# Kernel tuning notes

Measured on AMD Instinct MI355X. Metric: run time of the kernel, lower is better.

The kernel has to match this reference:

```python
import jax, jax.numpy as jnp
import numpy as np

B, T, DIM, NH = 2, 2048, 1024, 16
HD = DIM // NH  # 64


def setup_inputs() -> dict:
    key = jax.random.key(0)
    ks = jax.random.split(key, 5)
    x = jax.random.normal(ks[0], (B, T, DIM), dtype=jnp.float32)
    # realistic RoPE tables (any float tables work; use true rotary angles)
    inv_freq = 1.0 / (10000.0 ** (jnp.arange(0, HD, 2, dtype=jnp.float32) / HD))  # [HD/2]
    ang = jnp.arange(T, dtype=jnp.float32)[:, None] * inv_freq[None, :]           # [T, HD/2]
    ang = jnp.repeat(ang, 2, axis=-1)                                             # [T, HD] interleaved pairs
    sin = jnp.sin(ang)[None, None]  # [1,1,T,HD]
    cos = jnp.cos(ang)[None, None]
    W_qkv = jax.random.normal(ks[1], (DIM, 3 * DIM), dtype=jnp.float32) * (DIM ** -0.5)
    W_proj = jax.random.normal(ks[2], (DIM, DIM), dtype=jnp.float32) * (DIM ** -0.5)
    return {"x": x, "sin": sin, "cos": cos, "W_qkv": W_qkv, "W_proj": W_proj}


def _rope(x, sin, cos):
    # x: [B,H,T,D]; sin/cos: [1,1,T,D]
    x1, x2 = x[..., ::2], x[..., 1::2]
    xr = jnp.stack((-x2, x1), axis=-1).reshape(x.shape)  # interleave (-x2, x1)
    return x * cos + xr * sin


def reference(x, sin, cos, W_qkv, W_proj):
    Bx, Tx, C = x.shape
    nh, hd = NH, C // NH
    qkv = x @ W_qkv                                   # [B,T,3C]
    q, k, v = jnp.split(qkv, 3, axis=-1)
    to_bhtd = lambda t: t.reshape(Bx, Tx, nh, hd).transpose(0, 2, 1, 3)
    q, k, v = to_bhtd(q), to_bhtd(k), to_bhtd(v)      # [B,H,T,D]
    q = _rope(q, sin[:, :, :Tx], cos[:, :, :Tx])
    k = _rope(k, sin[:, :, :Tx], cos[:, :, :Tx])
    scale = 1.0 / jnp.sqrt(jnp.asarray(hd, dtype=x.dtype))
    scores = jnp.einsum('bhqd,bhkd->bhqk', q, k) * scale
    causal = jnp.tril(jnp.ones((Tx, Tx), dtype=bool))
    scores = jnp.where(causal, scores, jnp.finfo(scores.dtype).min)
    attn = jax.nn.softmax(scores, axis=-1)
    y = jnp.einsum('bhqk,bhkd->bhqd', attn, v)        # [B,H,T,D]
    y = y.transpose(0, 2, 1, 3).reshape(Bx, Tx, C)
    return y @ W_proj
```

## Files before the change

kernel.cpp:

```cpp
#include <hip/hip_runtime.h>


typedef float  f32x4   __attribute__((ext_vector_type(4)));
typedef float  f32x16  __attribute__((ext_vector_type(16)));
typedef __bf16 bf16x8  __attribute__((ext_vector_type(8)));
typedef short  short8  __attribute__((ext_vector_type(8)));
typedef unsigned uint2v __attribute__((ext_vector_type(2)));
typedef unsigned uint4v __attribute__((ext_vector_type(4)));

#define Bb   2
#define Tt   2048
#define DIMc 1024
#define NHh  16
#define HDd  64

__device__ __forceinline__ short f2bf(float f) {
    unsigned u = __builtin_bit_cast(unsigned, f);
    u += 0x7fffu + ((u >> 16) & 1u);
    return (short)(u >> 16);
}

__device__ __forceinline__ f32x4 mfma16(short8 a, short8 b, f32x4 c) {
    return __builtin_amdgcn_mfma_f32_16x16x32_bf16(
        __builtin_bit_cast(bf16x8, a), __builtin_bit_cast(bf16x8, b), c, 0, 0, 0);
}

__device__ __forceinline__ f32x16 mfma32(short8 a, short8 b, f32x16 c) {
    return __builtin_amdgcn_mfma_f32_32x32x16_bf16(
        __builtin_bit_cast(bf16x8, a), __builtin_bit_cast(bf16x8, b), c, 0, 0, 0);
}

__device__ __forceinline__ unsigned cvtpk(float lo, float hi) {
    unsigned r;
    asm("v_cvt_pk_bf16_f32 %0, %1, %2" : "=v"(r) : "v"(lo), "v"(hi));
    return r;
}

__device__ __forceinline__ void gl_lds16(const void* g, void* l) {
    __builtin_amdgcn_global_load_lds(
        (const __attribute__((address_space(1))) unsigned int*)g,
        (__attribute__((address_space(3))) unsigned int*)l, 16, 0, 0);
}

__global__ __launch_bounds__(256) void convX(const float* __restrict__ X,
                                             short* __restrict__ Xb)
{
    size_t i = ((size_t)blockIdx.x * 256 + threadIdx.x) * 8;
    float4 a = *(const float4*)(X + i);
    float4 b = *(const float4*)(X + i + 4);
    short8 s;
    s[0] = f2bf(a.x); s[1] = f2bf(a.y); s[2] = f2bf(a.z); s[3] = f2bf(a.w);
    s[4] = f2bf(b.x); s[5] = f2bf(b.y); s[6] = f2bf(b.z); s[7] = f2bf(b.w);
    *(short8*)(Xb + i) = s;
}

__global__ __launch_bounds__(256) void convT(const float* __restrict__ W,
                                             short* __restrict__ Wt, int N)
{
    __shared__ float L[64][65];
    const int kb = blockIdx.x * 64, nb = blockIdx.y * 64;
    const int tid = threadIdx.x;
#pragma unroll
    for (int it = 0; it < 4; it++) {
        int kk = it * 16 + (tid >> 4), c = (tid & 15) * 4;
        float4 v = *(const float4*)(W + (size_t)(kb + kk) * N + nb + c);
        L[c + 0][kk] = v.x; L[c + 1][kk] = v.y;
        L[c + 2][kk] = v.z; L[c + 3][kk] = v.w;
    }
    __syncthreads();
#pragma unroll
    for (int it = 0; it < 2; it++) {
        int n = it * 32 + (tid >> 3), ks = (tid & 7) * 8;
        short8 s;
#pragma unroll
        for (int j = 0; j < 8; j++) s[j] = f2bf(L[n][ks + j]);
        *(short8*)(Wt + (size_t)(nb + n) * 1024 + kb + ks) = s;
    }
}

__global__ __launch_bounds__(256, 6) void qkv_rope(
    const short* __restrict__ A, const short* __restrict__ Bt,
    const float* __restrict__ Sn, const float* __restrict__ Cs,
    short* __restrict__ Qo, short* __restrict__ Ko, short* __restrict__ Vt)
{
    __shared__ __align__(16) short LP[64 * 64 + 128 * 64];
    short (*As)[64] = (short(*)[64])LP;
    short (*Bs)[64] = (short(*)[64])(LP + 64 * 64);

    const int bm = blockIdx.x, bn = blockIdx.y;
    const int tid = threadIdx.x;
    const int wv = tid >> 6, lane = tid & 63, g = lane >> 4, l16 = lane & 15;
    const int wr = wv >> 1, wc = wv & 1;
    const int sw = l16 & 7;

    f32x4 acc[2][4];
#pragma unroll
    for (int i = 0; i < 2; i++)
#pragma unroll
        for (int j = 0; j < 4; j++) acc[i][j] = (f32x4){0.f, 0.f, 0.f, 0.f};

    const int sr = tid >> 3, c8 = tid & 7;
    const int gc8 = (c8 ^ (sr & 7)) << 3;
    const short* pA = A  + (size_t)(bm * 64  + sr) * 1024 + gc8;
    const short* pB = Bt + (size_t)(bn * 128 + sr) * 1024 + gc8;

    for (int k0 = 0; k0 < 1024; k0 += 64) {
        gl_lds16(pA + k0,             &As[sr][c8 << 3]);
        gl_lds16(pA + k0 + 32 * 1024, &As[32 + sr][c8 << 3]);
        gl_lds16(pB + k0,             &Bs[sr][c8 << 3]);
        gl_lds16(pB + k0 + 32 * 1024, &Bs[32 + sr][c8 << 3]);
        gl_lds16(pB + k0 + 64 * 1024, &Bs[64 + sr][c8 << 3]);
        gl_lds16(pB + k0 + 96 * 1024, &Bs[96 + sr][c8 << 3]);
        __syncthreads();
#pragma unroll
        for (int ks = 0; ks < 2; ks++) {
            short8 af[2], bfr[4];
#pragma unroll
            for (int mt = 0; mt < 2; mt++)
                af[mt]  = *(const short8*)&As[wr * 32 + mt * 16 + l16][((ks * 4 + g) ^ sw) << 3];
#pragma unroll
            for (int nt = 0; nt < 4; nt++)
                bfr[nt] = *(const short8*)&Bs[wc * 64 + nt * 16 + l16][((ks * 4 + g) ^ sw) << 3];
#pragma unroll
            for (int mt = 0; mt < 2; mt++)
#pragma unroll
                for (int nt = 0; nt < 4; nt++) acc[mt][nt] = mfma16(af[mt], bfr[nt], acc[mt][nt]);
        }
        __syncthreads();
    }

    if (bn >= 16) {
        short (*T)[72] = (short(*)[72])LP;
        const int b  = bm >> 5;
        const int t0 = (bm * 64) & 2047;
        const int nbase = (bn - 16) * 128;
#pragma unroll
        for (int ch = 0; ch < 4; ++ch) {
            __syncthreads();
            if (wc == (ch >> 1)) {
#pragma unroll
                for (int ntl = 0; ntl < 2; ++ntl) {
                    int nt = (ch & 1) * 2 + ntl;
#pragma unroll
                    for (int mt = 0; mt < 2; ++mt)
#pragma unroll
                        for (int r = 0; r < 4; ++r)
                            T[ntl * 16 + l16][wr * 32 + mt * 16 + g * 4 + r] =
                                f2bf(acc[mt][nt][r]);
                }
            }
            __syncthreads();
            int row = tid >> 3, cc8 = (tid & 7) * 8;
            int nn = nbase + ch * 32 + row;
            int h = nn >> 6, d = nn & 63;
            short8 v0 = *(const short8*)&T[row][cc8];
            size_t base = (((size_t)(b * 16 + h) * 64 + d) << 11) + t0 + cc8;
            *(short8*)(Vt + base) = v0;
        }
    } else {
#pragma unroll
        for (int mt = 0; mt < 2; mt++)
#pragma unroll
            for (int nt = 0; nt < 4; nt++)
#pragma unroll
                for (int r = 0; r < 4; r++) {
                    int m = bm * 64 + wr * 32 + mt * 16 + g * 4 + r;
                    int n = bn * 128 + wc * 64 + nt * 16 + l16;
                    float val = acc[mt][nt][r];
                    float partner = __shfl_xor(val, 1, 64);
                    int b = m >> 11, t = m & 2047;
                    int sec = n >> 10, nn = n & 1023;
                    int h = nn >> 6, d = nn & 63;
                    float sv = Sn[t * 64 + d], cv = Cs[t * 64 + d];
                    float ro = (d & 1) ? fmaf(val, cv, partner * sv)
                                       : fmaf(val, cv, -partner * sv);
                    short* dst = (sec == 0) ? Qo : Ko;
                    dst[(((size_t)(b * 16 + h) << 11) + t) * 64 + d] = f2bf(ro);
                }
    }
}

__global__ __launch_bounds__(64, 4) void attn(
    const short* __restrict__ Q, const short* __restrict__ K,
    const short* __restrict__ V, short* __restrict__ Y)
{
    const int id = blockIdx.x;
    const int bh = id >> 6;
    const int qw = ((id & 63) + ((id >> 8) << 3)) & 63;
    const int lane = threadIdx.x;
    const int l5 = lane & 31, hi = lane >> 5;
    const int q0 = qw * 32;
    const int qabs = q0 + l5;

    const short* Qb = Q + (size_t)bh * Tt * 64;
    const short* Kb = K + (size_t)bh * Tt * 64;
    const short* Vb = V + (size_t)bh * 64 * Tt;

    short8 qf[4];
#pragma unroll
    for (int c = 0; c < 4; c++)
        qf[c] = *(const short8*)(Qb + (size_t)(q0 + l5) * 64 + c * 16 + hi * 8);

    f32x16 o0, o1;
    float lsum = 0.f;
#pragma unroll
    for (int r = 0; r < 16; r++) { o0[r] = 0.f; o1[r] = 0.f; }

    const int nsteps = qw + 1;
    for (int s = 0; s < nsteps; ++s) {
        const int k0 = s * 32;
        const short* kp = Kb + (size_t)(k0 + l5) * 64 + hi * 8;
        short8 kf0 = *(const short8*)(kp);
        short8 kf1 = *(const short8*)(kp + 16);
        short8 kf2 = *(const short8*)(kp + 32);
        short8 kf3 = *(const short8*)(kp + 48);
        const short* vp = Vb + (size_t)l5 * Tt + k0 + hi * 8;
        short8 vf00 = *(const short8*)(vp);
        short8 vf01 = *(const short8*)(vp + 16);
        short8 vf10 = *(const short8*)(vp + 32 * Tt);
        short8 vf11 = *(const short8*)(vp + 32 * Tt + 16);

        f32x16 st;
#pragma unroll
        for (int r = 0; r < 16; r++) st[r] = 0.f;
        st = mfma32(kf0, qf[0], st);
        st = mfma32(kf1, qf[1], st);
        st = mfma32(kf2, qf[2], st);
        st = mfma32(kf3, qf[3], st);

        float p[16];
        if (s < nsteps - 1) {
#pragma unroll
            for (int r = 0; r < 16; r++)
                p[r] = __expf(fmaf(st[r], 0.125f, -10.f));
        } else {
#pragma unroll
            for (int r = 0; r < 16; r++) {
                int key = k0 + (r & 3) + 8 * (r >> 2) + 4 * hi;
                p[r] = (key <= qabs) ? __expf(fmaf(st[r], 0.125f, -10.f)) : 0.f;
            }
        }
#pragma unroll
        for (int r = 0; r < 16; r += 4)
            lsum += (p[r] + p[r + 1]) + (p[r + 2] + p[r + 3]);

        unsigned w[8];
#pragma unroll
        for (int t = 0; t < 4; t++) {
            w[2 * t]     = cvtpk(p[4 * t],     p[4 * t + 1]);
            w[2 * t + 1] = cvtpk(p[4 * t + 2], p[4 * t + 3]);
        }
        uint2v s0 = __builtin_amdgcn_permlane32_swap(w[0], w[2], false, false);
        uint2v s1 = __builtin_amdgcn_permlane32_swap(w[1], w[3], false, false);
        uint2v s2 = __builtin_amdgcn_permlane32_swap(w[4], w[6], false, false);
        uint2v s3 = __builtin_amdgcn_permlane32_swap(w[5], w[7], false, false);
        uint4v u0 = {s0[0], s1[0], s0[1], s1[1]};
        uint4v u1 = {s2[0], s3[0], s2[1], s3[1]};
        short8 pa0 = __builtin_bit_cast(short8, u0);
        short8 pa1 = __builtin_bit_cast(short8, u1);

        o0 = mfma32(pa0, vf00, o0);
        o0 = mfma32(pa1, vf01, o0);
        o1 = mfma32(pa0, vf10, o1);
        o1 = mfma32(pa1, vf11, o1);
    }

    lsum += __shfl_xor(lsum, 32, 64);
    float inv = 1.0f / lsum;
    const int b = bh >> 4, h = bh & 15;
#pragma unroll
    for (int r = 0; r < 16; r++) {
        int ql = (r & 3) + 8 * (r >> 2) + 4 * hi;
        float iv = __shfl(inv, ql, 64);
        size_t row = ((size_t)(b * Tt + q0 + ql)) * DIMc + h * 64;
        Y[row + l5]      = f2bf(o0[r] * iv);
        Y[row + 32 + l5] = f2bf(o1[r] * iv);
    }
}

__global__ __launch_bounds__(256, 4) void proj(
    const short* __restrict__ A, const short* __restrict__ Bt, float* __restrict__ O)
{
    __shared__ __align__(16) short As[64][64];
    __shared__ __align__(16) short Bs[64][64];
    const int bm = blockIdx.x, bn = blockIdx.y;
    const int tid = threadIdx.x;
    const int wv = tid >> 6, lane = tid & 63, g = lane >> 4, l16 = lane & 15;
    const int wr = wv >> 1, wc = wv & 1;
    const int sw = l16 & 7;

    f32x4 acc[2][2];
#pragma unroll
    for (int i = 0; i < 2; i++)
#pragma unroll
        for (int j = 0; j < 2; j++) acc[i][j] = (f32x4){0.f, 0.f, 0.f, 0.f};

    const int sr = tid >> 3, c8 = tid & 7;
    const int gc8 = (c8 ^ (sr & 7)) << 3;
    const short* pA = A  + (size_t)(bm * 64 + sr) * 1024 + gc8;
    const short* pB = Bt + (size_t)(bn * 64 + sr) * 1024 + gc8;

    for (int k0 = 0; k0 < 1024; k0 += 64) {
        gl_lds16(pA + k0,             &As[sr][c8 << 3]);
        gl_lds16(pA + k0 + 32 * 1024, &As[32 + sr][c8 << 3]);
        gl_lds16(pB + k0,             &Bs[sr][c8 << 3]);
        gl_lds16(pB + k0 + 32 * 1024, &Bs[32 + sr][c8 << 3]);
        __syncthreads();
#pragma unroll
        for (int ks = 0; ks < 2; ks++) {
            short8 af[2], bfr[2];
#pragma unroll
            for (int mt = 0; mt < 2; mt++)
                af[mt]  = *(const short8*)&As[wr * 32 + mt * 16 + l16][((ks * 4 + g) ^ sw) << 3];
#pragma unroll
            for (int nt = 0; nt < 2; nt++)
                bfr[nt] = *(const short8*)&Bs[wc * 32 + nt * 16 + l16][((ks * 4 + g) ^ sw) << 3];
#pragma unroll
            for (int mt = 0; mt < 2; mt++)
#pragma unroll
                for (int nt = 0; nt < 2; nt++) acc[mt][nt] = mfma16(af[mt], bfr[nt], acc[mt][nt]);
        }
        __syncthreads();
    }

#pragma unroll
    for (int mt = 0; mt < 2; mt++)
#pragma unroll
        for (int nt = 0; nt < 2; nt++)
#pragma unroll
            for (int r = 0; r < 4; r++) {
                int m = bm * 64 + wr * 32 + mt * 16 + g * 4 + r;
                int n = bn * 64 + wc * 32 + nt * 16 + l16;
                O[(size_t)m * 1024 + n] = acc[mt][nt][r];
            }
}

extern "C" void kernel_launch(void* const* d_in, const int* in_sizes, int n_in,
                              void* d_out, int out_size, void* d_ws, size_t ws_size,
                              hipStream_t stream)
{
    const float* x     = (const float*)d_in[0];
    const float* sn    = (const float*)d_in[1];
    const float* cs    = (const float*)d_in[2];
    const float* wqkv  = (const float*)d_in[3];
    const float* wproj = (const float*)d_in[4];
    float* out = (float*)d_out;

    char* ws = (char*)d_ws;
    const size_t MB = 1024 * 1024;
    short* q   = (short*)(ws);
    short* k   = (short*)(ws + 8  * MB);
    short* vt  = (short*)(ws + 16 * MB);
    short* y   = (short*)(ws + 24 * MB);
    short* xb  = (short*)(ws + 32 * MB);
    short* wqt = (short*)(ws + 40 * MB);
    short* wpt = (short*)(ws + 46 * MB);

    convX<<<2048, 256, 0, stream>>>(x, xb);
    convT<<<dim3(16, 48), 256, 0, stream>>>(wqkv, wqt, 3072);
    convT<<<dim3(16, 16), 256, 0, stream>>>(wproj, wpt, 1024);
    qkv_rope<<<dim3(64, 24), 256, 0, stream>>>(xb, wqt, sn, cs, q, k, vt);
    attn<<<dim3(Tt / 32 * Bb * NHh), 64, 0, stream>>>(q, k, vt, y);
    proj<<<dim3(64, 16), 256, 0, stream>>>(y, wpt, out);
}
```

Before: 220.9 us.

## Share K/V tiles in LDS across four waves with balanced causal pairing

```diff
diff --git a/kernel.cpp b/kernel.cpp
--- a/kernel.cpp
+++ b/kernel.cpp
@@ -180,102 +180,142 @@
     }
 }
 
-__global__ __launch_bounds__(64, 4) void attn(
+__global__ __launch_bounds__(256, 2) void attn(
     const short* __restrict__ Q, const short* __restrict__ K,
     const short* __restrict__ V, short* __restrict__ Y)
 {
-    const int id = blockIdx.x;
-    const int bh = id >> 6;
-    const int qw = ((id & 63) + ((id >> 8) << 3)) & 63;
-    const int lane = threadIdx.x;
+    __shared__ __align__(16) short Ks[2][64][64];
+    __shared__ __align__(16) short Vs[2][64][64];
+
+    const int bid = blockIdx.x;
+    const int xcd = bid & 7, idx = bid >> 3;
+    const int bh = xcd * 4 + (idx >> 4);
+    const int qb = idx & 15;
+    const int tid = threadIdx.x;
+    const int wv = tid >> 6, lane = tid & 63;
     const int l5 = lane & 31, hi = lane >> 5;
-    const int q0 = qw * 32;
-    const int qabs = q0 + l5;
+    const int swl = l5 & 7;
 
     const short* Qb = Q + (size_t)bh * Tt * 64;
     const short* Kb = K + (size_t)bh * Tt * 64;
     const short* Vb = V + (size_t)bh * 64 * Tt;
-
-    short8 qf[4];
-#pragma unroll
-    for (int c = 0; c < 4; c++)
-        qf[c] = *(const short8*)(Qb + (size_t)(q0 + l5) * 64 + c * 16 + hi * 8);
-
-    f32x16 o0, o1;
-    float lsum = 0.f;
-#pragma unroll
-    for (int r = 0; r < 16; r++) { o0[r] = 0.f; o1[r] = 0.f; }
-
-    const int nsteps = qw + 1;
-    for (int s = 0; s < nsteps; ++s) {
-        const int k0 = s * 32;
-        const short* kp = Kb + (size_t)(k0 + l5) * 64 + hi * 8;
-        short8 kf0 = *(const short8*)(kp);
-        short8 kf1 = *(const short8*)(kp + 16);
-        short8 kf2 = *(const short8*)(kp + 32);
-        short8 kf3 = *(const short8*)(kp + 48);
-        const short* vp = Vb + (size_t)l5 * Tt + k0 + hi * 8;
-        short8 vf00 = *(const short8*)(vp);
-        short8 vf01 = *(const short8*)(vp + 16);
-        short8 vf10 = *(const short8*)(vp + 32 * Tt);
-        short8 vf11 = *(const short8*)(vp + 32 * Tt + 16);
-
-        f32x16 st;
-#pragma unroll
-        for (int r = 0; r < 16; r++) st[r] = 0.f;
-        st = mfma32(kf0, qf[0], st);
-        st = mfma32(kf1, qf[1], st);
-        st = mfma32(kf2, qf[2], st);
-        st = mfma32(kf3, qf[3], st);
-
-        float p[16];
-        if (s < nsteps - 1) {
-#pragma unroll
-            for (int r = 0; r < 16; r++)
-                p[r] = __expf(fmaf(st[r], 0.125f, -10.f));
-        } else {
-#pragma unroll
-            for (int r = 0; r < 16; r++) {
-                int key = k0 + (r & 3) + 8 * (r >> 2) + 4 * hi;
-                p[r] = (key <= qabs) ? __expf(fmaf(st[r], 0.125f, -10.f)) : 0.f;
+    const int b = bh >> 4, h = bh & 15;
+
+    const int srow0 = wv * 16 + (lane >> 3);
+    const int sgp   = lane & 7;
+
+    auto stage = [&](int s, int buf) {
+        const int k0 = s * 64;
+#pragma unroll
+        for (int j = 0; j < 2; j++) {
+            int row = srow0 + j * 8;
+            int gl = sgp ^ (row & 7);
+            gl_lds16(Kb + (size_t)(k0 + row) * 64 + gl * 8, &Ks[buf][row][sgp << 3]);
+            gl_lds16(Vb + (size_t)row * Tt + k0 + gl * 8,   &Vs[buf][row][sgp << 3]);
+        }
+    };
+
+    auto run_phase = [&](int qw, int smax_blk) {
+        const int q0 = qw * 32, qabs = q0 + l5;
+        const int smax_w = qw >> 1;
+
+        short8 qf[4];
+#pragma unroll
+        for (int c = 0; c < 4; c++)
+            qf[c] = *(const short8*)(Qb + (size_t)(q0 + l5) * 64 + c * 16 + hi * 8);
+
+        f32x16 o0, o1;
+        float lsum = 0.f;
+#pragma unroll
+        for (int r = 0; r < 16; r++) { o0[r] = 0.f; o1[r] = 0.f; }
+
+        stage(0, 0);
+        __syncthreads();
+        for (int s = 0; s <= smax_blk; ++s) {
+            if (s < smax_blk) stage(s + 1, (s + 1) & 1);
+            if (s <= smax_w) {
+                const int buf = s & 1, k0 = s * 64;
+                short8 kfa[4], kfb[4];
+#pragma unroll
+                for (int dg = 0; dg < 4; dg++) {
+                    kfa[dg] = *(const short8*)&Ks[buf][l5]     [((((dg << 1) | hi)) ^ swl) << 3];
+                    kfb[dg] = *(const short8*)&Ks[buf][32 + l5][((((dg << 1) | hi)) ^ swl) << 3];
+                }
+                f32x16 sa, sb;
+#pragma unroll
+                for (int r = 0; r < 16; r++) { sa[r] = 0.f; sb[r] = 0.f; }
+#pragma unroll
+                for (int dg = 0; dg < 4; dg++) {
+                    sa = mfma32(kfa[dg], qf[dg], sa);
+                    sb = mfma32(kfb[dg], qf[dg], sb);
+                }
+                float pA[16], pB[16];
+                if (s < smax_w) {
+#pragma unroll
+                    for (int r = 0; r < 16; r++) {
+                        pA[r] = __expf(fmaf(sa[r], 0.125f, -10.f));
+                        pB[r] = __expf(fmaf(sb[r], 0.125f, -10.f));
+                    }
+                } else {
+#pragma unroll
+                    for (int r = 0; r < 16; r++) {
+                        int ka = k0 + (r & 3) + 8 * (r >> 2) + 4 * hi;
+                        pA[r] = (ka      <= qabs) ? __expf(fmaf(sa[r], 0.125f, -10.f)) : 0.f;
+                        pB[r] = (ka + 32 <= qabs) ? __expf(fmaf(sb[r], 0.125f, -10.f)) : 0.f;
+                    }
+                }
+#pragma unroll
+                for (int r = 0; r < 16; r += 4)
+                    lsum += ((pA[r] + pA[r + 1]) + (pA[r + 2] + pA[r + 3]))
+                          + ((pB[r] + pB[r + 1]) + (pB[r + 2] + pB[r + 3]));
+
+                unsigned wA[8], wB[8];
+#pragma unroll
+                for (int t = 0; t < 4; t++) {
+                    wA[2 * t]     = cvtpk(pA[4 * t],     pA[4 * t + 1]);
+                    wA[2 * t + 1] = cvtpk(pA[4 * t + 2], pA[4 * t + 3]);
+                    wB[2 * t]     = cvtpk(pB[4 * t],     pB[4 * t + 1]);
+                    wB[2 * t + 1] = cvtpk(pB[4 * t + 2], pB[4 * t + 3]);
+                }
+                uint2v a0 = __builtin_amdgcn_permlane32_swap(wA[0], wA[2], false, false);
+                uint2v a1 = __builtin_amdgcn_permlane32_swap(wA[1], wA[3], false, false);
+                uint2v a2 = __builtin_amdgcn_permlane32_swap(wA[4], wA[6], false, false);
+                uint2v a3 = __builtin_amdgcn_permlane32_swap(wA[5], wA[7], false, false);
+                uint2v b0 = __builtin_amdgcn_permlane32_swap(wB[0], wB[2], false, false);
+                uint2v b1 = __builtin_amdgcn_permlane32_swap(wB[1], wB[3], false, false);
+                uint2v b2 = __builtin_amdgcn_permlane32_swap(wB[4], wB[6], false, false);
+                uint2v b3 = __builtin_amdgcn_permlane32_swap(wB[5], wB[7], false, false);
+                short8 pav[4];
+                { uint4v u = {a0[0], a1[0], a0[1], a1[1]}; pav[0] = __builtin_bit_cast(short8, u); }
+                { uint4v u = {a2[0], a3[0], a2[1], a3[1]}; pav[1] = __builtin_bit_cast(short8, u); }
+                { uint4v u = {b0[0], b1[0], b0[1], b1[1]}; pav[2] = __builtin_bit_cast(short8, u); }
+                { uint4v u = {b2[0], b3[0], b2[1], b3[1]}; pav[3] = __builtin_bit_cast(short8, u); }
+
+#pragma unroll
+                for (int ks = 0; ks < 4; ks++) {
+                    short8 vf0 = *(const short8*)&Vs[buf][l5]     [((((ks << 1) | hi)) ^ swl) << 3];
+                    short8 vf1 = *(const short8*)&Vs[buf][32 + l5][((((ks << 1) | hi)) ^ swl) << 3];
+                    o0 = mfma32(pav[ks], vf0, o0);
+                    o1 = mfma32(pav[ks], vf1, o1);
+                }
             }
-        }
-#pragma unroll
-        for (int r = 0; r < 16; r += 4)
-            lsum += (p[r] + p[r + 1]) + (p[r + 2] + p[r + 3]);
-
-        unsigned w[8];
-#pragma unroll
-        for (int t = 0; t < 4; t++) {
-            w[2 * t]     = cvtpk(p[4 * t],     p[4 * t + 1]);
-            w[2 * t + 1] = cvtpk(p[4 * t + 2], p[4 * t + 3]);
-        }
-        uint2v s0 = __builtin_amdgcn_permlane32_swap(w[0], w[2], false, false);
-        uint2v s1 = __builtin_amdgcn_permlane32_swap(w[1], w[3], false, false);
-        uint2v s2 = __builtin_amdgcn_permlane32_swap(w[4], w[6], false, false);
-        uint2v s3 = __builtin_amdgcn_permlane32_swap(w[5], w[7], false, false);
-        uint4v u0 = {s0[0], s1[0], s0[1], s1[1]};
-        uint4v u1 = {s2[0], s3[0], s2[1], s3[1]};
-        short8 pa0 = __builtin_bit_cast(short8, u0);
-        short8 pa1 = __builtin_bit_cast(short8, u1);
-
-        o0 = mfma32(pa0, vf00, o0);
-        o0 = mfma32(pa1, vf01, o0);
-        o1 = mfma32(pa0, vf10, o1);
-        o1 = mfma32(pa1, vf11, o1);
-    }
-
-    lsum += __shfl_xor(lsum, 32, 64);
-    float inv = 1.0f / lsum;
-    const int b = bh >> 4, h = bh & 15;
-#pragma unroll
-    for (int r = 0; r < 16; r++) {
-        int ql = (r & 3) + 8 * (r >> 2) + 4 * hi;
-        float iv = __shfl(inv, ql, 64);
-        size_t row = ((size_t)(b * Tt + q0 + ql)) * DIMc + h * 64;
-        Y[row + l5]      = f2bf(o0[r] * iv);
-        Y[row + 32 + l5] = f2bf(o1[r] * iv);
-    }
+            __syncthreads();
+        }
+
+        lsum += __shfl_xor(lsum, 32, 64);
+        float inv = 1.0f / lsum;
+#pragma unroll
+        for (int r = 0; r < 16; r++) {
+            int ql = (r & 3) + 8 * (r >> 2) + 4 * hi;
+            float iv = __shfl(inv, ql, 64);
+            size_t row = ((size_t)(b * Tt + q0 + ql)) * DIMc + h * 64;
+            Y[row + l5]      = f2bf(o0[r] * iv);
+            Y[row + 32 + l5] = f2bf(o1[r] * iv);
+        }
+    };
+
+    run_phase(qb * 4 + wv, 2 * qb + 1);
+    run_phase(63 - qb * 4 - wv, 31 - 2 * qb);
 }
 
 __global__ __launch_bounds__(256, 4) void proj(
@@ -360,6 +400,6 @@
     convT<<<dim3(16, 48), 256, 0, stream>>>(wqkv, wqt, 3072);
     convT<<<dim3(16, 16), 256, 0, stream>>>(wproj, wpt, 1024);
     qkv_rope<<<dim3(64, 24), 256, 0, stream>>>(xb, wqt, sn, cs, q, k, vt);
-    attn<<<dim3(Tt / 32 * Bb * NHh), 64, 0, stream>>>(q, k, vt, y);
+    attn<<<dim3(512), 256, 0, stream>>>(q, k, vt, y);
     proj<<<dim3(64, 16), 256, 0, stream>>>(y, wpt, out);
 }
```

Result: faster. 191.0 us (-13.6%).
